# Kernel optimization log

Hardware: AMD Instinct MI355X
Metric: run time of the kernel (lower is better)

The kernel has to match this reference:

```python
import jax, jax.numpy as jnp
import numpy as np

H, DK, DV = 4, 64, 64        # heads, key/value head dims (hidden=256)
M, TOPK = 4, 2               # num memories, router top-k
GN, EPS, COND_SCALE = 16.0, 1e-5, 1.0


def setup_inputs() -> dict:
    key = jax.random.key(0)
    ks = jax.random.split(key, 12)
    B, Q, K, D = 8, 64, 256, 256
    w = lambda k, shape, fan: jax.random.normal(k, shape, jnp.float32) / np.sqrt(fan).astype(np.float32)
    return {
        "query": jax.random.normal(ks[0], (B, Q, D), jnp.float32),
        "keyval": jax.random.normal(ks[1], (B, K, D), jnp.float32),
        "attention_mask_kv": jnp.ones((B, K), jnp.int32),
        "W_cond": w(ks[2], (D, D), D),
        "W_q": w(ks[3], (D, H * DK), D),
        "W_k": w(ks[4], (D, H * DK), D),
        "W_v": w(ks[5], (D, H * DV), D),
        "W_gk1": w(ks[6], (D, 16), D),
        "W_gk2": w(ks[7], (16, H * DK), 16),
        "b_gk2": jnp.zeros((H * DK,), jnp.float32),
        "W_router": w(ks[8], (D, M), D),
        "norm_w": jnp.ones((DV,), jnp.float32),
        "W_o": w(ks[9], (H * DV, D), H * DV),
    }


def _mem_last(q_last, k, v, gk, sel, wgt):
    """Last-token output of one gated linear-attention memory.
    S_t = diag(exp(gk_t)) S_{t-1} + k_t v_t^T ; o_T = q_T S_T.
    q_last: (N,H,DK); k,gk: (N,K,H,DK); v: (N,K,H,DV); sel,wgt: (N,K)."""
    k_e = k * sel[:, :, None, None]
    v_e = v * wgt[:, :, None, None]
    gk_e = gk * sel[:, :, None, None]          # unselected tokens: no decay, no update
    G = jnp.cumsum(gk_e, axis=1)               # (N,K,H,DK), log decays
    decay = jnp.exp(G[:, -1:, :, :] - G)       # remaining decay to last step, <= 1
    s = jnp.einsum('nhd,nthd->nth', q_last, k_e * decay)
    return jnp.einsum('nth,nthv->nhv', s, v_e)


def reference(query, keyval, attention_mask_kv, W_cond, W_q, W_k, W_v,
              W_gk1, W_gk2, b_gk2, W_router, norm_w, W_o):
    B, Q, D = query.shape
    K = keyval.shape[1]
    N = B * Q
    # broadcast KV expansion + cond injection
    cond = (query @ W_cond) * COND_SCALE                         # (B,Q,D)
    x = (keyval[:, None, :, :] + cond[:, :, None, :]).reshape(N, K, D)
    m = jnp.broadcast_to(attention_mask_kv[:, None, :].astype(x.dtype), (B, Q, K)).reshape(N, K)
    # projections
    q = (x @ W_q).reshape(N, K, H, DK)
    k = (x @ W_k).reshape(N, K, H, DK) * m[:, :, None, None]
    v = (x @ W_v).reshape(N, K, H, DV) * m[:, :, None, None]
    gk = (jax.nn.log_sigmoid(x @ W_gk1 @ W_gk2 + b_gk2) / GN).reshape(N, K, H, DK)
    gk = gk * m[:, :, None, None]
    # router: softmax -> top-k -> renormalize
    router_logits = (x @ W_router).reshape(N * K, M)
    probs = jax.nn.softmax(router_logits, axis=-1)
    topv, topi = jax.lax.top_k(probs, TOPK)
    topv = topv / jnp.sum(topv, axis=-1, keepdims=True)
    w_mem = jnp.sum(jax.nn.one_hot(topi, M, dtype=x.dtype) * topv[..., None], axis=-2)
    w_mem = w_mem.reshape(N, K, M)
    # shared memory (always on) + routed memories
    q_last = q[:, -1]
    ones = jnp.ones((N, K), x.dtype)
    o = _mem_last(q_last, k, v, gk, ones, ones)
    for e in range(M):
        we = w_mem[:, :, e]
        o = o + _mem_last(q_last, k, v, gk, (we > 0).astype(x.dtype), we)
    # per-head RMSNorm + output projection
    o = o * jax.lax.rsqrt(jnp.mean(o * o, axis=-1, keepdims=True) + EPS) * norm_w
    out = (o.reshape(N, H * DV) @ W_o).reshape(B, Q, D)
    return out, router_logits
```

## Files before the change

### kernel.cpp

```cpp
#include <hip/hip_runtime.h>
#include <math.h>

#define Hh   4
#define DKk  64
#define DVv  64
#define Mm   4
#define Bb   8
#define Qq   64
#define Kk   256
#define Dd   256
#define Nn   (Bb * Qq)
#define GNf  16.0f
#define EPSf 1e-5f
#define WB   1088

__device__ __forceinline__ float wred(float x) {
#pragma unroll
    for (int off = 32; off > 0; off >>= 1)
        x += __shfl_xor(x, off, 64);
    return x;
}

__global__ __launch_bounds__(256) void pack_wb(
    const float* __restrict__ Wq, const float* __restrict__ Wk,
    const float* __restrict__ Wv, const float* __restrict__ Wg1,
    const float* __restrict__ Wg2, const float* __restrict__ Wr,
    float* __restrict__ Wb)
{
    const int idx = blockIdx.x * 256 + threadIdx.x;
    const int k = idx / WB, j = idx % WB;
    float v;
    if (j < 256)       v = Wq[(size_t)k * 256 + j];
    else if (j < 512)  v = Wk[(size_t)k * 256 + j - 256];
    else if (j < 768)  v = Wv[(size_t)k * 256 + j - 512];
    else if (j < 1024) {
        const int c = j - 768;
        float s = 0.f;
#pragma unroll
        for (int i = 0; i < 16; ++i)
            s = fmaf(Wg1[(size_t)k * 16 + i], Wg2[(size_t)i * 256 + c], s);
        v = s;
    }
    else if (j < 1028) v = Wr[(size_t)k * 4 + (j - 1024)];
    else               v = 0.f;
    Wb[idx] = v;
}

__global__ __launch_bounds__(256) void gemm_f32(
    const float* __restrict__ A, int lda, const float* __restrict__ W,
    float* __restrict__ C, int Nc, int Kc)
{
    __shared__ float As[64][17];
    __shared__ float Ws[16][65];
    const int tid = threadIdx.x;
    const int bm = blockIdx.y * 64;
    const int bn = blockIdx.x * 64;
    const int ty = tid >> 4, tx = tid & 15;
    const int aRow = tid >> 2;
    const int aCol = (tid & 3) * 4;
    const int wRow = tid >> 6;
    const int wCol = tid & 63;

    float acc[4][4] = {};

    for (int k0 = 0; k0 < Kc; k0 += 16) {
        const float4 av = *(const float4*)(A + (size_t)(bm + aRow) * lda + k0 + aCol);
        As[aRow][aCol + 0] = av.x;
        As[aRow][aCol + 1] = av.y;
        As[aRow][aCol + 2] = av.z;
        As[aRow][aCol + 3] = av.w;
#pragma unroll
        for (int r = 0; r < 4; ++r)
            Ws[wRow + 4 * r][wCol] = W[(size_t)(k0 + wRow + 4 * r) * Nc + bn + wCol];
        __syncthreads();
#pragma unroll
        for (int kk = 0; kk < 16; ++kk) {
            float a[4], wv[4];
#pragma unroll
            for (int i = 0; i < 4; ++i) a[i] = As[ty * 4 + i][kk];
#pragma unroll
            for (int j = 0; j < 4; ++j) wv[j] = Ws[kk][tx * 4 + j];
#pragma unroll
            for (int i = 0; i < 4; ++i)
#pragma unroll
                for (int j = 0; j < 4; ++j)
                    acc[i][j] = fmaf(a[i], wv[j], acc[i][j]);
        }
        __syncthreads();
    }

#pragma unroll
    for (int i = 0; i < 4; ++i)
#pragma unroll
        for (int j = 0; j < 4; ++j)
            C[(size_t)(bm + ty * 4 + i) * Nc + bn + tx * 4 + j] = acc[i][j];
}

__global__ __launch_bounds__(256) void mom_fused(
    const float* __restrict__ query, const float* __restrict__ W_cond,
    const float* __restrict__ Wb,    const float* __restrict__ b_gk2,
    const float* __restrict__ KVb,   const int* __restrict__ mask,
    const float* __restrict__ W_o,   const float* __restrict__ norm_w,
    float* __restrict__ out, float* __restrict__ logits)
{
    __shared__ float  qrow[256];
    __shared__ float  crow[256];
    __shared__ float4 wm[256];
    __shared__ float  rc4[4];
    __shared__ float  onorm[256];

    const int n = blockIdx.x;
    const int b = n >> 6;
    const int j = threadIdx.x;
    const int lane = j & 63;
    const int wv = j >> 6;

    qrow[j] = query[(size_t)n * Dd + j];
    __syncthreads();
    {
        float acc = 0.f;
#pragma unroll 8
        for (int k = 0; k < Dd; ++k)
            acc = fmaf(qrow[k], W_cond[(size_t)k * Dd + j], acc);
        crow[j] = acc;
    }
    __syncthreads();

    float qc = 0.f, kc = 0.f, vc = 0.f, pc = 0.f;
#pragma unroll 4
    for (int k = 0; k < Dd; ++k) {
        const float a = crow[k];
        const float* wp = Wb + (size_t)k * WB + j;
        qc = fmaf(a, wp[0],   qc);
        kc = fmaf(a, wp[256], kc);
        vc = fmaf(a, wp[512], vc);
        pc = fmaf(a, wp[768], pc);
    }
    pc += b_gk2[j];

    {
        float r = 0.f;
#pragma unroll
        for (int i = 0; i < 4; ++i) {
            const int k = lane + 64 * i;
            r = fmaf(crow[k], Wb[(size_t)k * WB + 1024 + wv], r);
        }
        r = wred(r);
        if (lane == 0) rc4[wv] = r;
    }
    __syncthreads();

    {
        const float4 kvr = *(const float4*)(KVb + (size_t)(b * Kk + j) * WB + 1024);
        float l[4] = {kvr.x + rc4[0], kvr.y + rc4[1], kvr.z + rc4[2], kvr.w + rc4[3]};
        *(float4*)(logits + ((size_t)n * Kk + j) * 4) = make_float4(l[0], l[1], l[2], l[3]);

        int i1 = 0;
#pragma unroll
        for (int q = 1; q < 4; ++q) if (l[q] > l[i1]) i1 = q;
        int i2 = -1;
#pragma unroll
        for (int q = 0; q < 4; ++q) {
            if (q == i1) continue;
            if (i2 < 0 || l[q] > l[i2]) i2 = q;
        }
        const float mx = fmaxf(l[i1], l[i2]);
        const float e1 = __expf(l[i1] - mx);
        const float e2 = __expf(l[i2] - mx);
        const float inv = 1.f / (e1 + e2);
        float w[4] = {0.f, 0.f, 0.f, 0.f};
        w[i1] = e1 * inv;
        w[i2] = e2 * inv;
        wm[j] = make_float4(w[0], w[1], w[2], w[3]);
    }
    __syncthreads();

    const float ql = KVb[(size_t)(b * Kk + Kk - 1) * WB + j] + qc;
    const float* pk = KVb + (size_t)b * Kk * WB + 256 + j;
    const float* pv = KVb + (size_t)b * Kk * WB + 512 + j;
    const float* pp = KVb + (size_t)b * Kk * WB + 768 + j;
    const int*   pm = mask + b * Kk;

    float E0 = 1.f, E1 = 1.f, E2 = 1.f, E3 = 1.f, E4 = 1.f;
    float o = 0.f;

#pragma unroll 4
    for (int t = Kk - 1; t >= 0; --t) {
        const float mf  = (float)pm[t];
        const float kk  = (pk[(size_t)t * WB] + kc) * mf;
        const float vv  = (pv[(size_t)t * WB] + vc) * mf;
        const float pre = pp[(size_t)t * WB] + pc;
        const float4 w  = wm[t];

        const float ls = fminf(pre, 0.f) - __logf(1.f + __expf(-fabsf(pre)));
        float dg = __expf(ls * (1.0f / GNf));
        dg = (mf != 0.f) ? dg : 1.f;

        const float zf = E0 + w.x * E1 + w.y * E2 + w.z * E3 + w.w * E4;
        const float s = wred(ql * kk * zf);
        o = fmaf(s, vv, o);

        E0 *= dg;
        E1 *= (w.x > 0.f) ? dg : 1.f;
        E2 *= (w.y > 0.f) ? dg : 1.f;
        E3 *= (w.z > 0.f) ? dg : 1.f;
        E4 *= (w.w > 0.f) ? dg : 1.f;
    }

    const float ms = wred(o * o) * (1.0f / 64.0f);
    onorm[j] = o * rsqrtf(ms + EPSf) * norm_w[lane];
    __syncthreads();

    {
        float acc = 0.f;
#pragma unroll 8
        for (int k = 0; k < Dd; ++k)
            acc = fmaf(onorm[k], W_o[(size_t)k * Dd + j], acc);
        out[(size_t)n * Dd + j] = acc;
    }
}

extern "C" void kernel_launch(void* const* d_in, const int* in_sizes, int n_in,
                              void* d_out, int out_size, void* d_ws, size_t ws_size,
                              hipStream_t stream)
{
    const float* query    = (const float*)d_in[0];
    const float* keyval   = (const float*)d_in[1];
    const int*   mask     = (const int*)  d_in[2];
    const float* W_cond   = (const float*)d_in[3];
    const float* W_q      = (const float*)d_in[4];
    const float* W_k      = (const float*)d_in[5];
    const float* W_v      = (const float*)d_in[6];
    const float* W_gk1    = (const float*)d_in[7];
    const float* W_gk2    = (const float*)d_in[8];
    const float* b_gk2    = (const float*)d_in[9];
    const float* W_router = (const float*)d_in[10];
    const float* norm_w   = (const float*)d_in[11];
    const float* W_o      = (const float*)d_in[12];

    float* out    = (float*)d_out;
    float* logits = out + Nn * Dd;

    float* p = (float*)d_ws;
    float* Wb  = p; p += Dd * WB;
    float* KVb = p; p += Bb * Kk * WB;

    pack_wb<<<(Dd * WB) / 256, dim3(256), 0, stream>>>(
        W_q, W_k, W_v, W_gk1, W_gk2, W_router, Wb);

    gemm_f32<<<dim3(WB / 64, (Bb * Kk) / 64), dim3(256), 0, stream>>>(
        keyval, Dd, Wb, KVb, WB, Dd);

    mom_fused<<<Nn, dim3(256), 0, stream>>>(
        query, W_cond, Wb, b_gk2, KVb, mask, W_o, norm_w, out, logits);
}
```

Before: 220.4 us.

## Batch cond projections into tiled GEMMs and chunk per-step reductions via LDS tiles

Moves the per-row query@W_cond and cond@Wb matrix-vector products out of the fused kernel into batched tiled GEMMs. The first GEMM is merged into the keyval GEMM launch, and the second is a separate launch writing a per-row Cb buffer. The recurrence loop now processes 16 timesteps per chunk: it stores per-step partial products into an LDS tile and reduces them together, which replaces one 64-lane shuffle reduction per step. This costs extra workspace, an extra launch, and global round-trips for the cond and Cb buffers.

```diff
diff --git a/kernel.cpp b/kernel.cpp
--- a/kernel.cpp
+++ b/kernel.cpp
@@ -2,9 +2,6 @@
 #include <math.h>
 
 #define Hh   4
-#define DKk  64
-#define DVv  64
-#define Mm   4
 #define Bb   8
 #define Qq   64
 #define Kk   256
@@ -46,9 +43,73 @@
     Wb[idx] = v;
 }
 
-__global__ __launch_bounds__(256) void gemm_f32(
-    const float* __restrict__ A, int lda, const float* __restrict__ W,
-    float* __restrict__ C, int Nc, int Kc)
+__global__ __launch_bounds__(256) void gemm1(
+    const float* __restrict__ keyval, const float* __restrict__ query,
+    const float* __restrict__ Wb, const float* __restrict__ W_cond,
+    float* __restrict__ KVb, float* __restrict__ cond)
+{
+    __shared__ float As[64][17];
+    __shared__ float Ws[16][65];
+    const int tid = threadIdx.x;
+
+    int id = blockIdx.x;
+    const float* A; const float* Bp; float* C;
+    int ldb, ldc;
+    if (id < 544) {
+        const int bm = (id / 17) * 64, bn = (id % 17) * 64;
+        A  = keyval + (size_t)bm * Dd;
+        Bp = Wb + bn;        ldb = WB;
+        C  = KVb + (size_t)bm * WB + bn;  ldc = WB;
+    } else {
+        id -= 544;
+        const int bm = (id >> 2) * 64, bn = (id & 3) * 64;
+        A  = query + (size_t)bm * Dd;
+        Bp = W_cond + bn;    ldb = Dd;
+        C  = cond + (size_t)bm * Dd + bn; ldc = Dd;
+    }
+
+    const int ty = tid >> 4, tx = tid & 15;
+    const int aRow = tid >> 2, aCol = (tid & 3) * 4;
+    const int wRow = tid >> 6, wCol = tid & 63;
+
+    float acc[4][4] = {};
+
+    for (int k0 = 0; k0 < Dd; k0 += 16) {
+        const float4 av = *(const float4*)(A + (size_t)aRow * Dd + k0 + aCol);
+        As[aRow][aCol + 0] = av.x;
+        As[aRow][aCol + 1] = av.y;
+        As[aRow][aCol + 2] = av.z;
+        As[aRow][aCol + 3] = av.w;
+#pragma unroll
+        for (int r = 0; r < 4; ++r)
+            Ws[wRow + 4 * r][wCol] = Bp[(size_t)(k0 + wRow + 4 * r) * ldb + wCol];
+        __syncthreads();
+#pragma unroll
+        for (int kk = 0; kk < 16; ++kk) {
+            float a[4], wv[4];
+#pragma unroll
+            for (int i = 0; i < 4; ++i) a[i] = As[ty * 4 + i][kk];
+#pragma unroll
+            for (int j = 0; j < 4; ++j) wv[j] = Ws[kk][tx * 4 + j];
+#pragma unroll
+            for (int i = 0; i < 4; ++i)
+#pragma unroll
+                for (int j = 0; j < 4; ++j)
+                    acc[i][j] = fmaf(a[i], wv[j], acc[i][j]);
+        }
+        __syncthreads();
+    }
+
+#pragma unroll
+    for (int i = 0; i < 4; ++i)
+#pragma unroll
+        for (int j = 0; j < 4; ++j)
+            C[(size_t)(ty * 4 + i) * ldc + tx * 4 + j] = acc[i][j];
+}
+
+__global__ __launch_bounds__(256) void gemm2(
+    const float* __restrict__ cond, const float* __restrict__ Wb,
+    float* __restrict__ Cb)
 {
     __shared__ float As[64][17];
     __shared__ float Ws[16][65];
@@ -56,22 +117,20 @@
     const int bm = blockIdx.y * 64;
     const int bn = blockIdx.x * 64;
     const int ty = tid >> 4, tx = tid & 15;
-    const int aRow = tid >> 2;
-    const int aCol = (tid & 3) * 4;
-    const int wRow = tid >> 6;
-    const int wCol = tid & 63;
+    const int aRow = tid >> 2, aCol = (tid & 3) * 4;
+    const int wRow = tid >> 6, wCol = tid & 63;
 
     float acc[4][4] = {};
 
-    for (int k0 = 0; k0 < Kc; k0 += 16) {
-        const float4 av = *(const float4*)(A + (size_t)(bm + aRow) * lda + k0 + aCol);
+    for (int k0 = 0; k0 < Dd; k0 += 16) {
+        const float4 av = *(const float4*)(cond + (size_t)(bm + aRow) * Dd + k0 + aCol);
         As[aRow][aCol + 0] = av.x;
         As[aRow][aCol + 1] = av.y;
         As[aRow][aCol + 2] = av.z;
         As[aRow][aCol + 3] = av.w;
 #pragma unroll
         for (int r = 0; r < 4; ++r)
-            Ws[wRow + 4 * r][wCol] = W[(size_t)(k0 + wRow + 4 * r) * Nc + bn + wCol];
+            Ws[wRow + 4 * r][wCol] = Wb[(size_t)(k0 + wRow + 4 * r) * WB + bn + wCol];
         __syncthreads();
 #pragma unroll
         for (int kk = 0; kk < 16; ++kk) {
@@ -93,21 +152,19 @@
     for (int i = 0; i < 4; ++i)
 #pragma unroll
         for (int j = 0; j < 4; ++j)
-            C[(size_t)(bm + ty * 4 + i) * Nc + bn + tx * 4 + j] = acc[i][j];
+            Cb[(size_t)(bm + ty * 4 + i) * WB + bn + tx * 4 + j] = acc[i][j];
 }
 
 __global__ __launch_bounds__(256) void mom_fused(
-    const float* __restrict__ query, const float* __restrict__ W_cond,
-    const float* __restrict__ Wb,    const float* __restrict__ b_gk2,
-    const float* __restrict__ KVb,   const int* __restrict__ mask,
-    const float* __restrict__ W_o,   const float* __restrict__ norm_w,
+    const float* __restrict__ KVb, const float* __restrict__ Cb,
+    const float* __restrict__ b_gk2, const int* __restrict__ mask,
+    const float* __restrict__ W_o, const float* __restrict__ norm_w,
     float* __restrict__ out, float* __restrict__ logits)
 {
-    __shared__ float  qrow[256];
-    __shared__ float  crow[256];
-    __shared__ float4 wm[256];
-    __shared__ float  rc4[4];
-    __shared__ float  onorm[256];
+    __shared__ float4 wm[Kk];
+    __shared__ float  Ptile[4][16][68];
+    __shared__ float  sbuf[4][16];
+    __shared__ float  onorm[Dd];
 
     const int n = blockIdx.x;
     const int b = n >> 6;
@@ -115,44 +172,15 @@
     const int lane = j & 63;
     const int wv = j >> 6;
 
-    qrow[j] = query[(size_t)n * Dd + j];
-    __syncthreads();
-    {
-        float acc = 0.f;
-#pragma unroll 8
-        for (int k = 0; k < Dd; ++k)
-            acc = fmaf(qrow[k], W_cond[(size_t)k * Dd + j], acc);
-        crow[j] = acc;
-    }
-    __syncthreads();
-
-    float qc = 0.f, kc = 0.f, vc = 0.f, pc = 0.f;
-#pragma unroll 4
-    for (int k = 0; k < Dd; ++k) {
-        const float a = crow[k];
-        const float* wp = Wb + (size_t)k * WB + j;
-        qc = fmaf(a, wp[0],   qc);
-        kc = fmaf(a, wp[256], kc);
-        vc = fmaf(a, wp[512], vc);
-        pc = fmaf(a, wp[768], pc);
-    }
-    pc += b_gk2[j];
-
-    {
-        float r = 0.f;
-#pragma unroll
-        for (int i = 0; i < 4; ++i) {
-            const int k = lane + 64 * i;
-            r = fmaf(crow[k], Wb[(size_t)k * WB + 1024 + wv], r);
-        }
-        r = wred(r);
-        if (lane == 0) rc4[wv] = r;
-    }
-    __syncthreads();
+    const float qc = Cb[(size_t)n * WB + j];
+    const float kc = Cb[(size_t)n * WB + 256 + j];
+    const float vc = Cb[(size_t)n * WB + 512 + j];
+    const float pc = Cb[(size_t)n * WB + 768 + j] + b_gk2[j];
+    const float4 rc = *(const float4*)(Cb + (size_t)n * WB + 1024);
 
     {
         const float4 kvr = *(const float4*)(KVb + (size_t)(b * Kk + j) * WB + 1024);
-        float l[4] = {kvr.x + rc4[0], kvr.y + rc4[1], kvr.z + rc4[2], kvr.w + rc4[3]};
+        float l[4] = {kvr.x + rc.x, kvr.y + rc.y, kvr.z + rc.z, kvr.w + rc.w};
         *(float4*)(logits + ((size_t)n * Kk + j) * 4) = make_float4(l[0], l[1], l[2], l[3]);
 
         int i1 = 0;
@@ -183,41 +211,64 @@
 
     float E0 = 1.f, E1 = 1.f, E2 = 1.f, E3 = 1.f, E4 = 1.f;
     float o = 0.f;
-
-#pragma unroll 4
-    for (int t = Kk - 1; t >= 0; --t) {
-        const float mf  = (float)pm[t];
-        const float kk  = (pk[(size_t)t * WB] + kc) * mf;
-        const float vv  = (pv[(size_t)t * WB] + vc) * mf;
-        const float pre = pp[(size_t)t * WB] + pc;
-        const float4 w  = wm[t];
-
-        const float ls = fminf(pre, 0.f) - __logf(1.f + __expf(-fabsf(pre)));
-        float dg = __expf(ls * (1.0f / GNf));
-        dg = (mf != 0.f) ? dg : 1.f;
-
-        const float zf = E0 + w.x * E1 + w.y * E2 + w.z * E3 + w.w * E4;
-        const float s = wred(ql * kk * zf);
-        o = fmaf(s, vv, o);
-
-        E0 *= dg;
-        E1 *= (w.x > 0.f) ? dg : 1.f;
-        E2 *= (w.y > 0.f) ? dg : 1.f;
-        E3 *= (w.z > 0.f) ? dg : 1.f;
-        E4 *= (w.w > 0.f) ? dg : 1.f;
+    const int tl = lane & 15, qq = lane >> 4;
+
+    for (int t0 = Kk - 16; t0 >= 0; t0 -= 16) {
+        float vreg[16];
+#pragma unroll
+        for (int i = 0; i < 16; ++i) {
+            const int t = t0 + 15 - i;
+            const float mf  = (float)pm[t];
+            const float kk  = (pk[(size_t)t * WB] + kc) * mf;
+            const float vvv = (pv[(size_t)t * WB] + vc) * mf;
+            const float pre = pp[(size_t)t * WB] + pc;
+            const float4 w  = wm[t];
+
+            const float ls = fminf(pre, 0.f) - __logf(1.f + __expf(-fabsf(pre)));
+            float dg = __expf(ls * (1.0f / GNf));
+            dg = (mf != 0.f) ? dg : 1.f;
+
+            const float zf = E0 + w.x * E1 + w.y * E2 + w.z * E3 + w.w * E4;
+            Ptile[wv][i][lane] = ql * kk * zf;
+            vreg[i] = vvv;
+
+            E0 *= dg;
+            E1 *= (w.x > 0.f) ? dg : 1.f;
+            E2 *= (w.y > 0.f) ? dg : 1.f;
+            E3 *= (w.z > 0.f) ? dg : 1.f;
+            E4 *= (w.w > 0.f) ? dg : 1.f;
+        }
+        __builtin_amdgcn_wave_barrier();
+
+        float s = 0.f;
+#pragma unroll
+        for (int r = 0; r < 4; ++r) {
+            const float4 p4 = *(const float4*)&Ptile[wv][tl][qq * 16 + r * 4];
+            s += (p4.x + p4.y) + (p4.z + p4.w);
+        }
+        s += __shfl_xor(s, 16, 64);
+        s += __shfl_xor(s, 32, 64);
+        sbuf[wv][tl] = s;
+        __builtin_amdgcn_wave_barrier();
+#pragma unroll
+        for (int r = 0; r < 4; ++r) {
+            const float4 sv = *(const float4*)&sbuf[wv][r * 4];
+            o = fmaf(sv.x, vreg[r * 4 + 0], o);
+            o = fmaf(sv.y, vreg[r * 4 + 1], o);
+            o = fmaf(sv.z, vreg[r * 4 + 2], o);
+            o = fmaf(sv.w, vreg[r * 4 + 3], o);
+        }
     }
 
     const float ms = wred(o * o) * (1.0f / 64.0f);
     onorm[j] = o * rsqrtf(ms + EPSf) * norm_w[lane];
     __syncthreads();
 
-    {
-        float acc = 0.f;
+    float acc = 0.f;
 #pragma unroll 8
-        for (int k = 0; k < Dd; ++k)
-            acc = fmaf(onorm[k], W_o[(size_t)k * Dd + j], acc);
-        out[(size_t)n * Dd + j] = acc;
-    }
+    for (int k = 0; k < Dd; ++k)
+        acc = fmaf(onorm[k], W_o[(size_t)k * Dd + j], acc);
+    out[(size_t)n * Dd + j] = acc;
 }
 
 extern "C" void kernel_launch(void* const* d_in, const int* in_sizes, int n_in,
@@ -242,15 +293,18 @@
     float* logits = out + Nn * Dd;
 
     float* p = (float*)d_ws;
-    float* Wb  = p; p += Dd * WB;
-    float* KVb = p; p += Bb * Kk * WB;
+    float* Wb   = p; p += Dd * WB;
+    float* KVb  = p; p += Bb * Kk * WB;
+    float* cond = p; p += Nn * Dd;
+    float* Cb   = p; p += Nn * WB;
 
     pack_wb<<<(Dd * WB) / 256, dim3(256), 0, stream>>>(
         W_q, W_k, W_v, W_gk1, W_gk2, W_router, Wb);
 
-    gemm_f32<<<dim3(WB / 64, (Bb * Kk) / 64), dim3(256), 0, stream>>>(
-        keyval, Dd, Wb, KVb, WB, Dd);
+    gemm1<<<576, dim3(256), 0, stream>>>(keyval, query, Wb, W_cond, KVb, cond);
+
+    gemm2<<<dim3(WB / 64, Nn / 64), dim3(256), 0, stream>>>(cond, Wb, Cb);
 
     mom_fused<<<Nn, dim3(256), 0, stream>>>(
-        query, W_cond, Wb, b_gk2, KVb, mask, W_o, norm_w, out, logits);
-}
+        KVb, Cb, b_gk2, mask, W_o, norm_w, out, logits);
+}
```

Measured after the change: 196.8 us. 1.12x faster.
